# Kernel tuning notes

Measured on AMD Instinct MI355X. Metric: run time of the kernel, lower is better.

## Reference

```python
import jax, jax.numpy as jnp
import numpy as np

N_NODES = 65536
N_EDGES = 1048576  # even: edges stored as interleaved reverse pairs
F_NODE = 133
F_EDGE = 14
HIDDEN = 128
DEPTH = 3
NUM_GRAPHS = 256


def setup_inputs() -> dict:
    key = jax.random.key(0)
    ks = jax.random.split(key, 10)
    x = jax.random.normal(ks[0], (N_NODES, F_NODE), dtype=jnp.float32)
    edge_attr = jax.random.normal(ks[1], (N_EDGES, F_EDGE), dtype=jnp.float32)
    # directed edges in reverse pairs: edge 2k = (u,v), edge 2k+1 = (v,u)
    src = jax.random.randint(ks[2], (N_EDGES // 2,), 0, N_NODES)
    dst = jax.random.randint(ks[3], (N_EDGES // 2,), 0, N_NODES)
    edge_index = jnp.stack([
        jnp.stack([src, dst], axis=1).reshape(-1),
        jnp.stack([dst, src], axis=1).reshape(-1),
    ]).astype(jnp.int64)
    batch = jnp.sort(jax.random.randint(ks[4], (N_NODES,), 0, NUM_GRAPHS)).astype(jnp.int64)
    def lin(k, fin, fout):
        return jax.random.normal(k, (fin, fout), dtype=jnp.float32) / np.sqrt(fin)
    We = lin(ks[5], F_NODE + F_EDGE, HIDDEN)
    be = jnp.zeros((HIDDEN,), dtype=jnp.float32)
    Wc = jax.random.normal(ks[6], (DEPTH, HIDDEN, HIDDEN), dtype=jnp.float32) / np.sqrt(HIDDEN)
    bc = jnp.zeros((DEPTH, HIDDEN), dtype=jnp.float32)
    Wn = lin(ks[7], F_NODE + HIDDEN, HIDDEN)
    bn = jnp.zeros((HIDDEN,), dtype=jnp.float32)
    return {"x": x, "edge_attr": edge_attr, "edge_index": edge_index, "batch": batch,
            "We": We, "be": be, "Wc": Wc, "bc": bc, "Wn": Wn, "bn": bn}


def reference(x, edge_attr, edge_index, batch, We, be, Wc, bc, Wn, bn):
    n_nodes = x.shape[0]
    row, col = edge_index[0], edge_index[1]
    # edge init: relu(Linear(cat(x[row], edge_attr)))
    h0 = jax.nn.relu(jnp.concatenate([x[row], edge_attr], axis=1) @ We + be)
    h = h0
    for l in range(DEPTH):
        # aggregate edge messages at target nodes (PyG add aggregation)
        agg = jax.ops.segment_sum(h, col, num_segments=n_nodes)
        # reverse-edge message: swap each consecutive pair
        rev = h.reshape(-1, 2, HIDDEN)[:, ::-1, :].reshape(-1, HIDDEN)
        h = (agg[row] - rev) @ Wc[l] + bc[l]
        h = jax.nn.relu(h + h0)  # residual then relu (dropout p used in eval = identity)
    # final aggregation to nodes using last conv (only aggregated message used)
    s = jax.ops.segment_sum(h, col, num_segments=n_nodes)
    q = jax.nn.relu(jnp.concatenate([x, s], axis=1) @ Wn + bn)
    # global_add_pool over graphs
    embedding = jax.ops.segment_sum(q, batch, num_segments=NUM_GRAPHS)
    return embedding
```

## Files before the change

kernel.cpp:

```cpp
#include <hip/hip_runtime.h>

#define N_NODES 65536
#define N_EDGES 1048576
#define F_NODE 133
#define F_EDGE 14
#define HID 128
#define GSTR 256

typedef __attribute__((ext_vector_type(4))) float f32x4;
typedef __attribute__((ext_vector_type(8))) short s16x8;
typedef __attribute__((ext_vector_type(4))) unsigned int u32x4;

__device__ __forceinline__ unsigned short f2bs(float f) {
  unsigned u = __float_as_uint(f);
  u += 0x7FFFu + ((u >> 16) & 1u);
  return (unsigned short)(u >> 16);
}
__device__ __forceinline__ unsigned pk2(float a, float b) {
  return (unsigned)f2bs(a) | ((unsigned)f2bs(b) << 16);
}
__device__ __forceinline__ float bflo(unsigned u) { return __uint_as_float(u << 16); }
__device__ __forceinline__ float bfhi(unsigned u) { return __uint_as_float(u & 0xffff0000u); }
__device__ __forceinline__ float bfs(unsigned short v) { return __uint_as_float((unsigned)v << 16); }

__device__ __forceinline__ int swz256(int row, int b) { return row * 256 + (b ^ ((row & 7) << 4)); }
__device__ __forceinline__ int swz64 (int row, int b) { return row * 64  + (b ^ ((row & 3) << 4)); }
__device__ __forceinline__ int swz384(int row, int b) { return row * 384 + (b ^ ((row & 7) << 4)); }

__global__ __launch_bounds__(256) void k_hist(const int* __restrict__ col, int* __restrict__ deg) {
  int e = blockIdx.x * 256 + threadIdx.x;
  atomicAdd(&deg[col[e]], 1);
}

__global__ __launch_bounds__(1024) void k_scan(const int* __restrict__ deg,
                                               int* __restrict__ base, int* __restrict__ cursor) {
  __shared__ int s0[1024], s1[1024];
  const int t = threadIdx.x;
  const int o = t * 64;
  int sum = 0;
  for (int i = 0; i < 64; ++i) sum += deg[o + i];
  s0[t] = sum;
  __syncthreads();
  int* src = s0; int* dst = s1;
  for (int off = 1; off < 1024; off <<= 1) {
    int v = src[t] + ((t >= off) ? src[t - off] : 0);
    dst[t] = v;
    __syncthreads();
    int* tmp = src; src = dst; dst = tmp;
  }
  int run = src[t] - sum;
  for (int i = 0; i < 64; ++i) {
    base[o + i] = run; cursor[o + i] = run;
    run += deg[o + i];
  }
  if (t == 1023) base[65536] = run;
}

__global__ __launch_bounds__(256) void k_fill(const int* __restrict__ col,
                                              int* __restrict__ cursor, int* __restrict__ eids) {
  int e = blockIdx.x * 256 + threadIdx.x;
  int pos = atomicAdd(&cursor[col[e]], 1);
  eids[pos] = e;
}

__global__ __launch_bounds__(256) void k_gather(
    const unsigned char* __restrict__ h8, const float* __restrict__ hscale,
    const int* __restrict__ base, const int* __restrict__ eids,
    unsigned short* __restrict__ G)
{
  const int tid = threadIdx.x;
  const int grp = tid >> 5, l = tid & 31;
  const int n = blockIdx.x * 8 + grp;
  const int s = base[n], E = base[n + 1];
  float a0 = 0.f, a1 = 0.f, a2 = 0.f, a3 = 0.f;
  int i = s;
  for (; i + 3 < E; i += 4) {
    int e0 = eids[i], e1 = eids[i + 1], e2 = eids[i + 2], e3 = eids[i + 3];
    unsigned q0 = *(const unsigned*)(h8 + (size_t)e0 * HID + l * 4);
    unsigned q1 = *(const unsigned*)(h8 + (size_t)e1 * HID + l * 4);
    unsigned q2 = *(const unsigned*)(h8 + (size_t)e2 * HID + l * 4);
    unsigned q3 = *(const unsigned*)(h8 + (size_t)e3 * HID + l * 4);
    float s0 = hscale[e0], s1 = hscale[e1], s2 = hscale[e2], s3 = hscale[e3];
    a0 += (float)(q0 & 255u) * s0 + (float)(q1 & 255u) * s1
        + (float)(q2 & 255u) * s2 + (float)(q3 & 255u) * s3;
    a1 += (float)((q0 >> 8) & 255u) * s0 + (float)((q1 >> 8) & 255u) * s1
        + (float)((q2 >> 8) & 255u) * s2 + (float)((q3 >> 8) & 255u) * s3;
    a2 += (float)((q0 >> 16) & 255u) * s0 + (float)((q1 >> 16) & 255u) * s1
        + (float)((q2 >> 16) & 255u) * s2 + (float)((q3 >> 16) & 255u) * s3;
    a3 += (float)(q0 >> 24) * s0 + (float)(q1 >> 24) * s1
        + (float)(q2 >> 24) * s2 + (float)(q3 >> 24) * s3;
  }
  for (; i < E; ++i) {
    int e0 = eids[i];
    unsigned q0 = *(const unsigned*)(h8 + (size_t)e0 * HID + l * 4);
    float s0 = hscale[e0];
    a0 += (float)(q0 & 255u) * s0;
    a1 += (float)((q0 >> 8) & 255u) * s0;
    a2 += (float)((q0 >> 16) & 255u) * s0;
    a3 += (float)(q0 >> 24) * s0;
  }
  uint2 wv;
  wv.x = pk2(a0, a1);
  wv.y = pk2(a2, a3);
  *(uint2*)(G + (size_t)n * GSTR + l * 4) = wv;
}

template<int MODE>
__global__ __launch_bounds__(256, 2) void k_fused(
    const unsigned short* __restrict__ G,
    const float* __restrict__ ea, const int* __restrict__ rowIdx,
    const float* __restrict__ We2, const float* __restrict__ be,
    const float* __restrict__ Wc, const float* __restrict__ bcL,
    unsigned char* __restrict__ h8, float* __restrict__ hscale)
{
  extern __shared__ char sm[];
  constexpr int WT_OFF  = 0;
  constexpr int WT2_OFF = MODE ? 32768 : 0;
  constexpr int M_OFF   = MODE ? 40960 : 0;
  constexpr int EA_OFF  = MODE ? 57344 : 8192;
  constexpr int BE_OFF  = MODE ? 61440 : 12288;
  constexpr int BC_OFF  = MODE ? 61952 : 12800;

  const int tid = threadIdx.x;
  const int lane = tid & 63, w = tid >> 6;
  const int g16 = lane >> 4, c16 = lane & 15;
  const int etM = tid >> 2;
  const int ccM = (tid & 3) * 32;

  u32x4 pG0, pG1, pG2, pG3;
  u32x4 pQa, pQb;
  float pS;
  float pEA0, pEA1, pEA2, pEA3;
  f32x4 pSeed[8];

  auto stage = [&](int EB) {
    if (MODE) {
      const int eM = EB + etM;
      const int rM = rowIdx[eM];
      const unsigned char* hp = h8 + (size_t)(eM ^ 1) * HID + ccM;
      pQa = *(const u32x4*)hp;
      pQb = *(const u32x4*)(hp + 16);
      pS = hscale[eM ^ 1];
      const u32x4* gp = (const u32x4*)(G + (size_t)rM * GSTR + ccM);
      pG0 = gp[0]; pG1 = gp[1]; pG2 = gp[2]; pG3 = gp[3];
    }
    {
      const float* eap = ea + (size_t)EB * F_EDGE;
      pEA0 = (tid < 896) ? eap[tid] : 0.f;
      pEA1 = (tid + 256 < 896) ? eap[tid + 256] : 0.f;
      pEA2 = (tid + 512 < 896) ? eap[tid + 512] : 0.f;
      pEA3 = (tid + 768 < 896) ? eap[tid + 768] : 0.f;
      const int er0n = EB + w * 16 + g16 * 4;
      const int rw0 = rowIdx[er0n], rw1 = rowIdx[er0n + 1];
      const int rw2 = rowIdx[er0n + 2], rw3 = rowIdx[er0n + 3];
      const unsigned short* x0 = G + (size_t)rw0 * GSTR + 128;
      const unsigned short* x1 = G + (size_t)rw1 * GSTR + 128;
      const unsigned short* x2 = G + (size_t)rw2 * GSTR + 128;
      const unsigned short* x3 = G + (size_t)rw3 * GSTR + 128;
#pragma unroll
      for (int jc = 0; jc < 8; ++jc) {
        const int j = jc * 16 + c16;
        pSeed[jc][0] = bfs(x0[j]);
        pSeed[jc][1] = bfs(x1[j]);
        pSeed[jc][2] = bfs(x2[j]);
        pSeed[jc][3] = bfs(x3[j]);
      }
    }
  };

  stage(blockIdx.x * 512);

  if (MODE) {
    for (int idx = tid; idx < HID * HID; idx += 256) {
      int k = idx >> 7, j = idx & 127;
      *(unsigned short*)(sm + WT_OFF + swz256(j, k * 2)) = f2bs(Wc[idx]);
    }
  }
  for (int idx = tid; idx < 32 * HID; idx += 256) {
    int k = idx >> 7, j = idx & 127;
    float v = (k < F_EDGE) ? We2[k * HID + j] : 0.f;
    *(unsigned short*)(sm + WT2_OFF + swz64(j, k * 2)) = f2bs(v);
  }
  for (int idx = tid; idx < 64 * 18; idx += 256) {
    int e_t = idx / 18, kz = 14 + idx % 18;
    *(unsigned short*)(sm + EA_OFF + swz64(e_t, kz * 2)) = 0;
  }
  if (tid < HID) {
    ((float*)(sm + BE_OFF))[tid] = be[tid];
    if (MODE) ((float*)(sm + BC_OFF))[tid] = bcL[tid];
  }

  for (int it = 0; it < 8; ++it) {
    const int e_base = (blockIdx.x * 8 + it) * 64;
    const int er0 = e_base + w * 16 + g16 * 4;

    f32x4 acc[8];
#pragma unroll
    for (int jc = 0; jc < 8; ++jc) acc[jc] = pSeed[jc];

    __syncthreads();

    if (tid < 896) {
      int e_t = tid / F_EDGE, k = tid - e_t * F_EDGE;
      *(unsigned short*)(sm + EA_OFF + swz64(e_t, k * 2)) = f2bs(pEA0);
    }
    if (tid + 256 < 896) {
      int i = tid + 256, e_t = i / F_EDGE, k = i - e_t * F_EDGE;
      *(unsigned short*)(sm + EA_OFF + swz64(e_t, k * 2)) = f2bs(pEA1);
    }
    if (tid + 512 < 896) {
      int i = tid + 512, e_t = i / F_EDGE, k = i - e_t * F_EDGE;
      *(unsigned short*)(sm + EA_OFF + swz64(e_t, k * 2)) = f2bs(pEA2);
    }
    if (tid + 768 < 896) {
      int i = tid + 768, e_t = i / F_EDGE, k = i - e_t * F_EDGE;
      *(unsigned short*)(sm + EA_OFF + swz64(e_t, k * 2)) = f2bs(pEA3);
    }
    if (MODE) {
      const float s = pS;
#define MW(GW, Q) pk2(bflo(GW) - (float)((Q) & 255u) * s, bfhi(GW) - (float)(((Q) >> 8) & 255u) * s)
      u32x4 v;
      v.x = MW(pG0.x, pQa.x); v.y = MW(pG0.y, pQa.x >> 16);
      v.z = MW(pG0.z, pQa.y); v.w = MW(pG0.w, pQa.y >> 16);
      *(u32x4*)(sm + M_OFF + swz256(etM, ccM * 2 +  0)) = v;
      v.x = MW(pG1.x, pQa.z); v.y = MW(pG1.y, pQa.z >> 16);
      v.z = MW(pG1.z, pQa.w); v.w = MW(pG1.w, pQa.w >> 16);
      *(u32x4*)(sm + M_OFF + swz256(etM, ccM * 2 + 16)) = v;
      v.x = MW(pG2.x, pQb.x); v.y = MW(pG2.y, pQb.x >> 16);
      v.z = MW(pG2.z, pQb.y); v.w = MW(pG2.w, pQb.y >> 16);
      *(u32x4*)(sm + M_OFF + swz256(etM, ccM * 2 + 32)) = v;
      v.x = MW(pG3.x, pQb.z); v.y = MW(pG3.y, pQb.z >> 16);
      v.z = MW(pG3.z, pQb.w); v.w = MW(pG3.w, pQb.w >> 16);
      *(u32x4*)(sm + M_OFF + swz256(etM, ccM * 2 + 48)) = v;
#undef MW
    }

    if (it < 7) stage(e_base + 64);

    __syncthreads();

    {
      const s16x8 afrag = *(const s16x8*)(sm + EA_OFF + swz64(w * 16 + c16, g16 * 16));
#pragma unroll
      for (int jc = 0; jc < 8; ++jc) {
        const s16x8 bf = *(const s16x8*)(sm + WT2_OFF + swz64(jc * 16 + c16, g16 * 16));
        acc[jc] = __builtin_amdgcn_mfma_f32_16x16x32_bf16(afrag, bf, acc[jc], 0, 0, 0);
      }
    }
#pragma unroll
    for (int jc = 0; jc < 8; ++jc) {
      const float bev = ((const float*)(sm + BE_OFF))[jc * 16 + c16];
      const float bcv = MODE ? ((const float*)(sm + BC_OFF))[jc * 16 + c16] : 0.f;
#pragma unroll
      for (int r = 0; r < 4; ++r) {
        float h0v = fmaxf(acc[jc][r] + bev, 0.f);
        acc[jc][r] = MODE ? (h0v + bcv) : h0v;
      }
    }
    if (MODE) {
#pragma unroll
      for (int kk = 0; kk < 4; ++kk) {
        const s16x8 am = *(const s16x8*)(sm + M_OFF + swz256(w * 16 + c16, kk * 64 + g16 * 16));
#pragma unroll
        for (int jc = 0; jc < 8; ++jc) {
          const s16x8 bf = *(const s16x8*)(sm + WT_OFF + swz256(jc * 16 + c16, kk * 64 + g16 * 16));
          acc[jc] = __builtin_amdgcn_mfma_f32_16x16x32_bf16(am, bf, acc[jc], 0, 0, 0);
        }
      }
#pragma unroll
      for (int jc = 0; jc < 8; ++jc)
#pragma unroll
        for (int r = 0; r < 4; ++r)
          acc[jc][r] = fmaxf(acc[jc][r], 0.f);
    }
    float inv[4], sc[4];
#pragma unroll
    for (int r = 0; r < 4; ++r) {
      float m = 0.f;
#pragma unroll
      for (int jc = 0; jc < 8; ++jc) m = fmaxf(m, acc[jc][r]);
#pragma unroll
      for (int off = 1; off < 16; off <<= 1)
        m = fmaxf(m, __shfl_xor(m, off, 64));
      sc[r]  = m > 0.f ? m * (1.f / 255.f) : 0.f;
      inv[r] = m > 0.f ? 255.f / m : 0.f;
    }
    if (c16 == 0) {
#pragma unroll
      for (int r = 0; r < 4; ++r) hscale[er0 + r] = sc[r];
    }
#pragma unroll
    for (int jc = 0; jc < 8; ++jc) {
      const int j = jc * 16 + c16;
      h8[(size_t)(er0 + 0) * HID + j] = (unsigned char)__float2uint_rn(fminf(acc[jc][0] * inv[0], 255.f));
      h8[(size_t)(er0 + 1) * HID + j] = (unsigned char)__float2uint_rn(fminf(acc[jc][1] * inv[1], 255.f));
      h8[(size_t)(er0 + 2) * HID + j] = (unsigned char)__float2uint_rn(fminf(acc[jc][2] * inv[2], 255.f));
      h8[(size_t)(er0 + 3) * HID + j] = (unsigned char)__float2uint_rn(fminf(acc[jc][3] * inv[3], 255.f));
    }
  }
}

template<int TOG>
__global__ __launch_bounds__(256) void k_prep(
    const float* __restrict__ x, const float* __restrict__ W,
    float* __restrict__ outf, unsigned short* __restrict__ G)
{
  extern __shared__ char sm[];
  char* WTp = sm;
  char* Ap  = sm + 49152;
  const int tid = threadIdx.x, lane = tid & 63, w = tid >> 6;
  const int g16 = lane >> 4, c16 = lane & 15;

  for (int idx = tid; idx < 192 * HID; idx += 256) {
    int k = idx >> 7, j = idx & 127;
    float v = (k < F_NODE) ? W[(size_t)k * HID + j] : 0.f;
    *(unsigned short*)(WTp + swz384(j, k * 2)) = f2bs(v);
  }
  for (int it = 0; it < 2; ++it) {
    const int nbase = (blockIdx.x * 2 + it) * 64;
    __syncthreads();
    for (int idx = tid; idx < 64 * 192; idx += 256) {
      int r = idx / 192, k = idx - r * 192;
      float v = (k < F_NODE) ? x[(size_t)(nbase + r) * F_NODE + k] : 0.f;
      *(unsigned short*)(Ap + swz384(r, k * 2)) = f2bs(v);
    }
    __syncthreads();
    f32x4 acc[8];
#pragma unroll
    for (int jc = 0; jc < 8; ++jc) acc[jc] = (f32x4)(0.f);
#pragma unroll
    for (int kk = 0; kk < 5; ++kk) {
      const s16x8 af = *(const s16x8*)(Ap + swz384(w * 16 + c16, kk * 64 + g16 * 16));
#pragma unroll
      for (int jc = 0; jc < 8; ++jc) {
        const s16x8 bf = *(const s16x8*)(WTp + swz384(jc * 16 + c16, kk * 64 + g16 * 16));
        acc[jc] = __builtin_amdgcn_mfma_f32_16x16x32_bf16(af, bf, acc[jc], 0, 0, 0);
      }
    }
    const int r0 = nbase + w * 16 + g16 * 4;
#pragma unroll
    for (int jc = 0; jc < 8; ++jc)
#pragma unroll
      for (int r = 0; r < 4; ++r) {
        if (TOG)
          G[(size_t)(r0 + r) * GSTR + 128 + jc * 16 + c16] = f2bs(acc[jc][r]);
        else
          outf[(size_t)(r0 + r) * HID + jc * 16 + c16] = acc[jc][r];
      }
  }
}

__global__ __launch_bounds__(256) void k_nodef(
    const unsigned short* __restrict__ G, const float* __restrict__ xwn,
    const float* __restrict__ WnS, const float* __restrict__ bn,
    const int* __restrict__ batch, float* __restrict__ out)
{
  extern __shared__ char sm[];
  char* WTp = sm;
  char* Ap  = sm + 32768;
  float* bnl = (float*)(sm + 49152);
  const int tid = threadIdx.x, lane = tid & 63, w = tid >> 6;
  const int g16 = lane >> 4, c16 = lane & 15;

  for (int idx = tid; idx < HID * HID; idx += 256) {
    int k = idx >> 7, j = idx & 127;
    *(unsigned short*)(WTp + swz256(j, k * 2)) = f2bs(WnS[(size_t)k * HID + j]);
  }
  if (tid < HID) bnl[tid] = bn[tid];

  for (int it = 0; it < 2; ++it) {
    const int nbase = (blockIdx.x * 2 + it) * 64;
    __syncthreads();
    {
      const int r = tid >> 2, cc = (tid & 3) * 32;
      const u32x4* gp = (const u32x4*)(G + (size_t)(nbase + r) * GSTR + cc);
      *(u32x4*)(Ap + swz256(r, cc * 2 +  0)) = gp[0];
      *(u32x4*)(Ap + swz256(r, cc * 2 + 16)) = gp[1];
      *(u32x4*)(Ap + swz256(r, cc * 2 + 32)) = gp[2];
      *(u32x4*)(Ap + swz256(r, cc * 2 + 48)) = gp[3];
    }
    __syncthreads();
    const int r0 = nbase + w * 16 + g16 * 4;
    f32x4 acc[8];
#pragma unroll
    for (int jc = 0; jc < 8; ++jc) {
      const float bv = bnl[jc * 16 + c16];
#pragma unroll
      for (int r = 0; r < 4; ++r)
        acc[jc][r] = xwn[(size_t)(r0 + r) * HID + jc * 16 + c16] + bv;
    }
#pragma unroll
    for (int kk = 0; kk < 4; ++kk) {
      const s16x8 af = *(const s16x8*)(Ap + swz256(w * 16 + c16, kk * 64 + g16 * 16));
#pragma unroll
      for (int jc = 0; jc < 8; ++jc) {
        const s16x8 bf = *(const s16x8*)(WTp + swz256(jc * 16 + c16, kk * 64 + g16 * 16));
        acc[jc] = __builtin_amdgcn_mfma_f32_16x16x32_bf16(af, bf, acc[jc], 0, 0, 0);
      }
    }
    const int b0 = batch[r0], b1 = batch[r0 + 1];
    const int b2 = batch[r0 + 2], b3 = batch[r0 + 3];
#pragma unroll
    for (int jc = 0; jc < 8; ++jc) {
      const int j = jc * 16 + c16;
      atomicAdd(&out[(size_t)b0 * HID + j], fmaxf(acc[jc][0], 0.f));
      atomicAdd(&out[(size_t)b1 * HID + j], fmaxf(acc[jc][1], 0.f));
      atomicAdd(&out[(size_t)b2 * HID + j], fmaxf(acc[jc][2], 0.f));
      atomicAdd(&out[(size_t)b3 * HID + j], fmaxf(acc[jc][3], 0.f));
    }
  }
}

__global__ void k_diag(float* out, int n, float v) {
  int i = blockIdx.x * 256 + threadIdx.x;
  if (i < n) out[i] = v;
}

extern "C" void kernel_launch(void* const* d_in, const int* in_sizes, int n_in,
                              void* d_out, int out_size, void* d_ws, size_t ws_size,
                              hipStream_t stream) {
  const float* x     = (const float*)d_in[0];
  const float* ea    = (const float*)d_in[1];
  const int*   ei    = (const int*)d_in[2];
  const int*   batch = (const int*)d_in[3];
  const float* We    = (const float*)d_in[4];
  const float* be    = (const float*)d_in[5];
  const float* Wc    = (const float*)d_in[6];
  const float* bc    = (const float*)d_in[7];
  const float* Wn    = (const float*)d_in[8];
  const float* bn    = (const float*)d_in[9];
  float* out = (float*)d_out;

  const int* row = ei;
  const int* col = ei + N_EDGES;
  const float* We2 = We + F_NODE * HID;
  const float* WnS = Wn + F_NODE * HID;

  const size_t szH8    = (size_t)N_EDGES * HID;
  const size_t szScale = (size_t)N_EDGES * sizeof(float);
  const size_t szG     = (size_t)N_NODES * GSTR * sizeof(short);
  const size_t szXwn   = (size_t)N_NODES * HID * sizeof(float);
  const size_t szEids  = (size_t)N_EDGES * sizeof(int);
  const size_t szDeg   = (size_t)N_NODES * sizeof(int);
  const size_t szBase  = ((size_t)(N_NODES + 1) * sizeof(int) + 255) & ~255ULL;

  size_t off = 0;
  char* ws = (char*)d_ws;
  unsigned char*  h8     = (unsigned char*)(ws + off);  off += szH8;
  float*          hscale = (float*)(ws + off);          off += szScale;
  unsigned short* G      = (unsigned short*)(ws + off); off += szG;
  float*          xwn    = (float*)(ws + off);          off += szXwn;
  int*            eids   = (int*)(ws + off);            off += szEids;
  int*            deg    = (int*)(ws + off);            off += szDeg;
  int*            base   = (int*)(ws + off);            off += szBase;
  int*            cursor = (int*)(ws + off);            off += szDeg;
  const size_t need = off;

  if (ws_size < need) {
    k_diag<<<(out_size + 255) / 256, 256, 0, stream>>>(out, out_size, (float)ws_size);
    return;
  }

  const size_t lds_f0 = 12800;
  const size_t lds_f1 = 62464;
  const size_t lds_pp = 49152 + 24576;
  const size_t lds_nf = 49152 + 512;

  (void)hipFuncSetAttribute((const void*)(k_fused<0>),
      hipFuncAttributeMaxDynamicSharedMemorySize, (int)lds_f0);
  (void)hipFuncSetAttribute((const void*)(k_fused<1>),
      hipFuncAttributeMaxDynamicSharedMemorySize, (int)lds_f1);
  (void)hipFuncSetAttribute((const void*)(k_prep<0>),
      hipFuncAttributeMaxDynamicSharedMemorySize, (int)lds_pp);
  (void)hipFuncSetAttribute((const void*)(k_prep<1>),
      hipFuncAttributeMaxDynamicSharedMemorySize, (int)lds_pp);
  (void)hipFuncSetAttribute((const void*)k_nodef,
      hipFuncAttributeMaxDynamicSharedMemorySize, (int)lds_nf);

  hipMemsetAsync(deg, 0, szDeg, stream);
  k_hist<<<N_EDGES / 256, 256, 0, stream>>>(col, deg);
  k_scan<<<1, 1024, 0, stream>>>(deg, base, cursor);
  k_fill<<<N_EDGES / 256, 256, 0, stream>>>(col, cursor, eids);

  k_prep<1><<<512, 256, lds_pp, stream>>>(x, We, nullptr, G);
  k_prep<0><<<512, 256, lds_pp, stream>>>(x, Wn, xwn, nullptr);

  k_fused<0><<<2048, 256, lds_f0, stream>>>(G, ea, row, We2, be,
                                            nullptr, nullptr, h8, hscale);

  for (int l = 0; l < 3; ++l) {
    k_gather<<<N_NODES / 8, 256, 0, stream>>>(h8, hscale, base, eids, G);
    k_fused<1><<<2048, 256, lds_f1, stream>>>(G, ea, row, We2, be,
                                              Wc + (size_t)l * HID * HID, bc + (size_t)l * HID,
                                              h8, hscale);
  }

  k_gather<<<N_NODES / 8, 256, 0, stream>>>(h8, hscale, base, eids, G);

  hipMemsetAsync(out, 0, (size_t)out_size * sizeof(float), stream);
  k_nodef<<<512, 256, lds_nf, stream>>>(G, xwn, WnS, bn, batch, out);
}
```

Measured before the change: 1.332 ms.

## Build edge-attr MFMA fragment in registers and shrink LDS for higher occupancy

Result: slower. 1.607 ms (+20.6%).

```diff
diff --git a/kernel.cpp b/kernel.cpp
--- a/kernel.cpp
+++ b/kernel.cpp
@@ -24,8 +24,8 @@
 __device__ __forceinline__ float bfs(unsigned short v) { return __uint_as_float((unsigned)v << 16); }
 
 __device__ __forceinline__ int swz256(int row, int b) { return row * 256 + (b ^ ((row & 7) << 4)); }
-__device__ __forceinline__ int swz64 (int row, int b) { return row * 64  + (b ^ ((row & 3) << 4)); }
 __device__ __forceinline__ int swz384(int row, int b) { return row * 384 + (b ^ ((row & 7) << 4)); }
+__device__ __forceinline__ int swz32 (int row, int b) { return row * 32  + (b ^ ((row & 1) << 4)); }
 
 __global__ __launch_bounds__(256) void k_hist(const int* __restrict__ col, int* __restrict__ deg) {
   int e = blockIdx.x * 256 + threadIdx.x;
@@ -106,7 +106,7 @@
 }
 
 template<int MODE>
-__global__ __launch_bounds__(256, 2) void k_fused(
+__global__ __launch_bounds__(256, 3) void k_fused(
     const unsigned short* __restrict__ G,
     const float* __restrict__ ea, const int* __restrict__ rowIdx,
     const float* __restrict__ We2, const float* __restrict__ be,
@@ -115,11 +115,8 @@
 {
   extern __shared__ char sm[];
   constexpr int WT_OFF  = 0;
-  constexpr int WT2_OFF = MODE ? 32768 : 0;
-  constexpr int M_OFF   = MODE ? 40960 : 0;
-  constexpr int EA_OFF  = MODE ? 57344 : 8192;
-  constexpr int BE_OFF  = MODE ? 61440 : 12288;
-  constexpr int BC_OFF  = MODE ? 61952 : 12800;
+  constexpr int M_OFF   = MODE ? 32768 : 0;
+  constexpr int WT2_OFF = MODE ? 49152 : 0;
 
   const int tid = threadIdx.x;
   const int lane = tid & 63, w = tid >> 6;
@@ -130,7 +127,7 @@
   u32x4 pG0, pG1, pG2, pG3;
   u32x4 pQa, pQb;
   float pS;
-  float pEA0, pEA1, pEA2, pEA3;
+  float2 pE0, pE1, pE2, pE3;
   f32x4 pSeed[8];
 
   auto stage = [&](int EB) {
@@ -145,11 +142,18 @@
       pG0 = gp[0]; pG1 = gp[1]; pG2 = gp[2]; pG3 = gp[3];
     }
     {
-      const float* eap = ea + (size_t)EB * F_EDGE;
-      pEA0 = (tid < 896) ? eap[tid] : 0.f;
-      pEA1 = (tid + 256 < 896) ? eap[tid + 256] : 0.f;
-      pEA2 = (tid + 512 < 896) ? eap[tid + 512] : 0.f;
-      pEA3 = (tid + 768 < 896) ? eap[tid + 768] : 0.f;
+      pE0 = make_float2(0.f, 0.f); pE1 = pE0; pE2 = pE0; pE3 = pE0;
+      const float* eap = ea + (size_t)(EB + w * 16 + c16) * F_EDGE;
+      if (g16 == 0) {
+        pE0 = *(const float2*)(eap + 0);
+        pE1 = *(const float2*)(eap + 2);
+        pE2 = *(const float2*)(eap + 4);
+        pE3 = *(const float2*)(eap + 6);
+      } else if (g16 == 1) {
+        pE0 = *(const float2*)(eap + 8);
+        pE1 = *(const float2*)(eap + 10);
+        pE2 = *(const float2*)(eap + 12);
+      }
       const int er0n = EB + w * 16 + g16 * 4;
       const int rw0 = rowIdx[er0n], rw1 = rowIdx[er0n + 1];
       const int rw2 = rowIdx[er0n + 2], rw3 = rowIdx[er0n + 3];
@@ -170,24 +174,24 @@
 
   stage(blockIdx.x * 512);
 
+  float bev[8], bcv[8];
+#pragma unroll
+  for (int jc = 0; jc < 8; ++jc) {
+    const int j = jc * 16 + c16;
+    bev[jc] = be[j];
+    bcv[jc] = MODE ? bcL[j] : 0.f;
+  }
+
   if (MODE) {
     for (int idx = tid; idx < HID * HID; idx += 256) {
       int k = idx >> 7, j = idx & 127;
       *(unsigned short*)(sm + WT_OFF + swz256(j, k * 2)) = f2bs(Wc[idx]);
     }
   }
-  for (int idx = tid; idx < 32 * HID; idx += 256) {
+  for (int idx = tid; idx < 16 * HID; idx += 256) {
     int k = idx >> 7, j = idx & 127;
     float v = (k < F_EDGE) ? We2[k * HID + j] : 0.f;
-    *(unsigned short*)(sm + WT2_OFF + swz64(j, k * 2)) = f2bs(v);
-  }
-  for (int idx = tid; idx < 64 * 18; idx += 256) {
-    int e_t = idx / 18, kz = 14 + idx % 18;
-    *(unsigned short*)(sm + EA_OFF + swz64(e_t, kz * 2)) = 0;
-  }
-  if (tid < HID) {
-    ((float*)(sm + BE_OFF))[tid] = be[tid];
-    if (MODE) ((float*)(sm + BC_OFF))[tid] = bcL[tid];
+    *(unsigned short*)(sm + WT2_OFF + swz32(j, k * 2)) = f2bs(v);
   }
 
   for (int it = 0; it < 8; ++it) {
@@ -198,24 +202,15 @@
 #pragma unroll
     for (int jc = 0; jc < 8; ++jc) acc[jc] = pSeed[jc];
 
-    __syncthreads();
-
-    if (tid < 896) {
-      int e_t = tid / F_EDGE, k = tid - e_t * F_EDGE;
-      *(unsigned short*)(sm + EA_OFF + swz64(e_t, k * 2)) = f2bs(pEA0);
-    }
-    if (tid + 256 < 896) {
-      int i = tid + 256, e_t = i / F_EDGE, k = i - e_t * F_EDGE;
-      *(unsigned short*)(sm + EA_OFF + swz64(e_t, k * 2)) = f2bs(pEA1);
-    }
-    if (tid + 512 < 896) {
-      int i = tid + 512, e_t = i / F_EDGE, k = i - e_t * F_EDGE;
-      *(unsigned short*)(sm + EA_OFF + swz64(e_t, k * 2)) = f2bs(pEA2);
-    }
-    if (tid + 768 < 896) {
-      int i = tid + 768, e_t = i / F_EDGE, k = i - e_t * F_EDGE;
-      *(unsigned short*)(sm + EA_OFF + swz64(e_t, k * 2)) = f2bs(pEA3);
-    }
+    u32x4 eau;
+    eau.x = pk2(pE0.x, pE0.y);
+    eau.y = pk2(pE1.x, pE1.y);
+    eau.z = pk2(pE2.x, pE2.y);
+    eau.w = pk2(pE3.x, pE3.y);
+    const s16x8 eafrag = *(const s16x8*)&eau;
+
+    __syncthreads();
+
     if (MODE) {
       const float s = pS;
 #define MW(GW, Q) pk2(bflo(GW) - (float)((Q) & 255u) * s, bfhi(GW) - (float)(((Q) >> 8) & 255u) * s)
@@ -240,21 +235,20 @@
     __syncthreads();
 
     {
-      const s16x8 afrag = *(const s16x8*)(sm + EA_OFF + swz64(w * 16 + c16, g16 * 16));
+      const int bo = (g16 & 2) ? 0 : (g16 << 4);
 #pragma unroll
       for (int jc = 0; jc < 8; ++jc) {
-        const s16x8 bf = *(const s16x8*)(sm + WT2_OFF + swz64(jc * 16 + c16, g16 * 16));
-        acc[jc] = __builtin_amdgcn_mfma_f32_16x16x32_bf16(afrag, bf, acc[jc], 0, 0, 0);
+        const int jrow = jc * 16 + c16;
+        const s16x8 bf = *(const s16x8*)(sm + WT2_OFF + swz32(jrow, bo));
+        acc[jc] = __builtin_amdgcn_mfma_f32_16x16x32_bf16(eafrag, bf, acc[jc], 0, 0, 0);
       }
     }
 #pragma unroll
     for (int jc = 0; jc < 8; ++jc) {
-      const float bev = ((const float*)(sm + BE_OFF))[jc * 16 + c16];
-      const float bcv = MODE ? ((const float*)(sm + BC_OFF))[jc * 16 + c16] : 0.f;
 #pragma unroll
       for (int r = 0; r < 4; ++r) {
-        float h0v = fmaxf(acc[jc][r] + bev, 0.f);
-        acc[jc][r] = MODE ? (h0v + bcv) : h0v;
+        float h0v = fmaxf(acc[jc][r] + bev[jc], 0.f);
+        acc[jc][r] = MODE ? (h0v + bcv[jc]) : h0v;
       }
     }
     if (MODE) {
@@ -461,8 +455,8 @@
     return;
   }
 
-  const size_t lds_f0 = 12800;
-  const size_t lds_f1 = 62464;
+  const size_t lds_f0 = 4096;
+  const size_t lds_f1 = 53248;
   const size_t lds_pp = 49152 + 24576;
   const size_t lds_nf = 49152 + 512;
 
```

## Store edge states in destination-sorted order so gather reads contiguously

Applied to the files above, without the earlier changes.

After: 1.303 ms. 1.02x faster.

```diff
diff --git a/kernel.cpp b/kernel.cpp
--- a/kernel.cpp
+++ b/kernel.cpp
@@ -57,16 +57,20 @@
 }
 
 __global__ __launch_bounds__(256) void k_fill(const int* __restrict__ col,
-                                              int* __restrict__ cursor, int* __restrict__ eids) {
+                                              int* __restrict__ cursor, int* __restrict__ invp) {
   int e = blockIdx.x * 256 + threadIdx.x;
   int pos = atomicAdd(&cursor[col[e]], 1);
-  eids[pos] = e;
+  invp[e] = pos;
+}
+
+__global__ __launch_bounds__(256) void k_revp(const int* __restrict__ invp, int* __restrict__ revp) {
+  int e = blockIdx.x * 256 + threadIdx.x;
+  revp[e] = invp[e ^ 1];
 }
 
 __global__ __launch_bounds__(256) void k_gather(
     const unsigned char* __restrict__ h8, const float* __restrict__ hscale,
-    const int* __restrict__ base, const int* __restrict__ eids,
-    unsigned short* __restrict__ G)
+    const int* __restrict__ base, unsigned short* __restrict__ G)
 {
   const int tid = threadIdx.x;
   const int grp = tid >> 5, l = tid & 31;
@@ -75,12 +79,11 @@
   float a0 = 0.f, a1 = 0.f, a2 = 0.f, a3 = 0.f;
   int i = s;
   for (; i + 3 < E; i += 4) {
-    int e0 = eids[i], e1 = eids[i + 1], e2 = eids[i + 2], e3 = eids[i + 3];
-    unsigned q0 = *(const unsigned*)(h8 + (size_t)e0 * HID + l * 4);
-    unsigned q1 = *(const unsigned*)(h8 + (size_t)e1 * HID + l * 4);
-    unsigned q2 = *(const unsigned*)(h8 + (size_t)e2 * HID + l * 4);
-    unsigned q3 = *(const unsigned*)(h8 + (size_t)e3 * HID + l * 4);
-    float s0 = hscale[e0], s1 = hscale[e1], s2 = hscale[e2], s3 = hscale[e3];
+    unsigned q0 = *(const unsigned*)(h8 + (size_t)i * HID + l * 4);
+    unsigned q1 = *(const unsigned*)(h8 + (size_t)(i + 1) * HID + l * 4);
+    unsigned q2 = *(const unsigned*)(h8 + (size_t)(i + 2) * HID + l * 4);
+    unsigned q3 = *(const unsigned*)(h8 + (size_t)(i + 3) * HID + l * 4);
+    float s0 = hscale[i], s1 = hscale[i + 1], s2 = hscale[i + 2], s3 = hscale[i + 3];
     a0 += (float)(q0 & 255u) * s0 + (float)(q1 & 255u) * s1
         + (float)(q2 & 255u) * s2 + (float)(q3 & 255u) * s3;
     a1 += (float)((q0 >> 8) & 255u) * s0 + (float)((q1 >> 8) & 255u) * s1
@@ -91,9 +94,8 @@
         + (float)(q2 >> 24) * s2 + (float)(q3 >> 24) * s3;
   }
   for (; i < E; ++i) {
-    int e0 = eids[i];
-    unsigned q0 = *(const unsigned*)(h8 + (size_t)e0 * HID + l * 4);
-    float s0 = hscale[e0];
+    unsigned q0 = *(const unsigned*)(h8 + (size_t)i * HID + l * 4);
+    float s0 = hscale[i];
     a0 += (float)(q0 & 255u) * s0;
     a1 += (float)((q0 >> 8) & 255u) * s0;
     a2 += (float)((q0 >> 16) & 255u) * s0;
@@ -109,6 +111,7 @@
 __global__ __launch_bounds__(256, 2) void k_fused(
     const unsigned short* __restrict__ G,
     const float* __restrict__ ea, const int* __restrict__ rowIdx,
+    const int* __restrict__ invp, const int* __restrict__ revp,
     const float* __restrict__ We2, const float* __restrict__ be,
     const float* __restrict__ Wc, const float* __restrict__ bcL,
     unsigned char* __restrict__ h8, float* __restrict__ hscale)
@@ -132,15 +135,17 @@
   float pS;
   float pEA0, pEA1, pEA2, pEA3;
   f32x4 pSeed[8];
+  int pI0, pI1, pI2, pI3;
 
   auto stage = [&](int EB) {
     if (MODE) {
       const int eM = EB + etM;
-      const int rM = rowIdx[eM];
-      const unsigned char* hp = h8 + (size_t)(eM ^ 1) * HID + ccM;
+      const int rp = revp[eM];
+      const unsigned char* hp = h8 + (size_t)rp * HID + ccM;
       pQa = *(const u32x4*)hp;
       pQb = *(const u32x4*)(hp + 16);
-      pS = hscale[eM ^ 1];
+      pS = hscale[rp];
+      const int rM = rowIdx[eM];
       const u32x4* gp = (const u32x4*)(G + (size_t)rM * GSTR + ccM);
       pG0 = gp[0]; pG1 = gp[1]; pG2 = gp[2]; pG3 = gp[3];
     }
@@ -151,6 +156,10 @@
       pEA2 = (tid + 512 < 896) ? eap[tid + 512] : 0.f;
       pEA3 = (tid + 768 < 896) ? eap[tid + 768] : 0.f;
       const int er0n = EB + w * 16 + g16 * 4;
+      pI0 = invp[er0n];
+      pI1 = invp[er0n + 1];
+      pI2 = invp[er0n + 2];
+      pI3 = invp[er0n + 3];
       const int rw0 = rowIdx[er0n], rw1 = rowIdx[er0n + 1];
       const int rw2 = rowIdx[er0n + 2], rw3 = rowIdx[er0n + 3];
       const unsigned short* x0 = G + (size_t)rw0 * GSTR + 128;
@@ -192,11 +201,11 @@
 
   for (int it = 0; it < 8; ++it) {
     const int e_base = (blockIdx.x * 8 + it) * 64;
-    const int er0 = e_base + w * 16 + g16 * 4;
 
     f32x4 acc[8];
 #pragma unroll
     for (int jc = 0; jc < 8; ++jc) acc[jc] = pSeed[jc];
+    const int cI0 = pI0, cI1 = pI1, cI2 = pI2, cI3 = pI3;
 
     __syncthreads();
 
@@ -286,16 +295,18 @@
       inv[r] = m > 0.f ? 255.f / m : 0.f;
     }
     if (c16 == 0) {
-#pragma unroll
-      for (int r = 0; r < 4; ++r) hscale[er0 + r] = sc[r];
+      hscale[cI0] = sc[0];
+      hscale[cI1] = sc[1];
+      hscale[cI2] = sc[2];
+      hscale[cI3] = sc[3];
     }
 #pragma unroll
     for (int jc = 0; jc < 8; ++jc) {
       const int j = jc * 16 + c16;
-      h8[(size_t)(er0 + 0) * HID + j] = (unsigned char)__float2uint_rn(fminf(acc[jc][0] * inv[0], 255.f));
-      h8[(size_t)(er0 + 1) * HID + j] = (unsigned char)__float2uint_rn(fminf(acc[jc][1] * inv[1], 255.f));
-      h8[(size_t)(er0 + 2) * HID + j] = (unsigned char)__float2uint_rn(fminf(acc[jc][2] * inv[2], 255.f));
-      h8[(size_t)(er0 + 3) * HID + j] = (unsigned char)__float2uint_rn(fminf(acc[jc][3] * inv[3], 255.f));
+      h8[(size_t)cI0 * HID + j] = (unsigned char)__float2uint_rn(fminf(acc[jc][0] * inv[0], 255.f));
+      h8[(size_t)cI1 * HID + j] = (unsigned char)__float2uint_rn(fminf(acc[jc][1] * inv[1], 255.f));
+      h8[(size_t)cI2 * HID + j] = (unsigned char)__float2uint_rn(fminf(acc[jc][2] * inv[2], 255.f));
+      h8[(size_t)cI3 * HID + j] = (unsigned char)__float2uint_rn(fminf(acc[jc][3] * inv[3], 255.f));
     }
   }
 }
@@ -440,7 +451,7 @@
   const size_t szScale = (size_t)N_EDGES * sizeof(float);
   const size_t szG     = (size_t)N_NODES * GSTR * sizeof(short);
   const size_t szXwn   = (size_t)N_NODES * HID * sizeof(float);
-  const size_t szEids  = (size_t)N_EDGES * sizeof(int);
+  const size_t szIdx   = (size_t)N_EDGES * sizeof(int);
   const size_t szDeg   = (size_t)N_NODES * sizeof(int);
   const size_t szBase  = ((size_t)(N_NODES + 1) * sizeof(int) + 255) & ~255ULL;
 
@@ -450,7 +461,8 @@
   float*          hscale = (float*)(ws + off);          off += szScale;
   unsigned short* G      = (unsigned short*)(ws + off); off += szG;
   float*          xwn    = (float*)(ws + off);          off += szXwn;
-  int*            eids   = (int*)(ws + off);            off += szEids;
+  int*            invp   = (int*)(ws + off);            off += szIdx;
+  int*            revp   = (int*)(ws + off);            off += szIdx;
   int*            deg    = (int*)(ws + off);            off += szDeg;
   int*            base   = (int*)(ws + off);            off += szBase;
   int*            cursor = (int*)(ws + off);            off += szDeg;
@@ -480,22 +492,23 @@
   hipMemsetAsync(deg, 0, szDeg, stream);
   k_hist<<<N_EDGES / 256, 256, 0, stream>>>(col, deg);
   k_scan<<<1, 1024, 0, stream>>>(deg, base, cursor);
-  k_fill<<<N_EDGES / 256, 256, 0, stream>>>(col, cursor, eids);
+  k_fill<<<N_EDGES / 256, 256, 0, stream>>>(col, cursor, invp);
+  k_revp<<<N_EDGES / 256, 256, 0, stream>>>(invp, revp);
 
   k_prep<1><<<512, 256, lds_pp, stream>>>(x, We, nullptr, G);
   k_prep<0><<<512, 256, lds_pp, stream>>>(x, Wn, xwn, nullptr);
 
-  k_fused<0><<<2048, 256, lds_f0, stream>>>(G, ea, row, We2, be,
+  k_fused<0><<<2048, 256, lds_f0, stream>>>(G, ea, row, invp, revp, We2, be,
                                             nullptr, nullptr, h8, hscale);
 
   for (int l = 0; l < 3; ++l) {
-    k_gather<<<N_NODES / 8, 256, 0, stream>>>(h8, hscale, base, eids, G);
-    k_fused<1><<<2048, 256, lds_f1, stream>>>(G, ea, row, We2, be,
+    k_gather<<<N_NODES / 8, 256, 0, stream>>>(h8, hscale, base, G);
+    k_fused<1><<<2048, 256, lds_f1, stream>>>(G, ea, row, invp, revp, We2, be,
                                               Wc + (size_t)l * HID * HID, bc + (size_t)l * HID,
                                               h8, hscale);
   }
 
-  k_gather<<<N_NODES / 8, 256, 0, stream>>>(h8, hscale, base, eids, G);
+  k_gather<<<N_NODES / 8, 256, 0, stream>>>(h8, hscale, base, G);
 
   hipMemsetAsync(out, 0, (size_t)out_size * sizeof(float), stream);
   k_nodef<<<512, 256, lds_nf, stream>>>(G, xwn, WnS, bn, batch, out);
```
